# Performance work log

Hardware: AMD Instinct MI355X
Metric: run time of the kernel (lower is better)

Reference implementation:

```python
import jax, jax.numpy as jnp
import numpy as np

L, H, NH, V, T, B, K = 12, 768, 12, 30522, 512, 4, 21
DH = H // NH
INV_SQRT_DH = 1.0 / float(np.sqrt(DH))
NEG = -1e4  # BERT additive mask value
LN_EPS = 1e-12


def _ln(x, g, b):
    m = x.mean(-1, keepdims=True)
    v = jnp.var(x, axis=-1, keepdims=True)
    return (x - m) * jax.lax.rsqrt(v + LN_EPS) * g + b


def _encoder(input_ids, attention_mask, word_emb, pos_emb, tok_emb, emb_g, emb_b,
             Wqkv, bqkv, Wo, bo, ln1_g, ln1_b, W1, b1, W2, b2, ln2_g, ln2_b):
    Bv, Tv = input_ids.shape
    h = word_emb[input_ids] + pos_emb[None, :Tv] + tok_emb[0]  # token_type_ids = 0
    h = _ln(h, emb_g, emb_b)
    bias = (1.0 - attention_mask[:, None, None, :].astype(h.dtype)) * NEG  # [B,1,1,T]

    def layer(h, xs):
        wqkv, bq, wo, bo_, g1, b1_, w1, bb1, w2, bb2, g2, b2_ = xs
        qkv = h @ wqkv + bq  # [B,T,3H]
        q, k, v = jnp.split(qkv, 3, axis=-1)
        def hd(x):
            return x.reshape(Bv, Tv, NH, DH).transpose(0, 2, 1, 3)
        q, k, v = hd(q), hd(k), hd(v)
        scores = jnp.einsum('bhqd,bhkd->bhqk', q, k) * INV_SQRT_DH + bias
        ctx = jnp.einsum('bhqk,bhkd->bhqd', jax.nn.softmax(scores, axis=-1), v)
        ctx = ctx.transpose(0, 2, 1, 3).reshape(Bv, Tv, H)
        h = _ln(h + ctx @ wo + bo_, g1, b1_)  # post-LN (BERT)
        ff = jax.nn.gelu(h @ w1 + bb1, approximate=False) @ w2 + bb2
        h = _ln(h + ff, g2, b2_)
        return h, None

    h, _ = jax.lax.scan(layer, h, (Wqkv, bqkv, Wo, bo, ln1_g, ln1_b, W1, b1, W2, b2, ln2_g, ln2_b))
    return h


def _crf_nll(emissions, tags, mask, start, end, trans):
    # emissions [B,T,K], tags [B,T] int, mask [B,T] bool; torchcrf reduction='mean'
    Bv, Tv, Kv = emissions.shape
    maskf = mask.astype(emissions.dtype)
    # numerator: score of the gold path
    num = start[tags[:, 0]] + emissions[jnp.arange(Bv), 0, tags[:, 0]]
    em_t = jnp.take_along_axis(emissions, tags[..., None], axis=-1)[..., 0]  # [B,T]
    tr_t = trans[tags[:, :-1], tags[:, 1:]]  # [B,T-1]
    num = num + jnp.sum((tr_t + em_t[:, 1:]) * maskf[:, 1:], axis=1)
    last_idx = mask.sum(axis=1).astype(jnp.int32) - 1
    last_tag = jnp.take_along_axis(tags, last_idx[:, None], axis=1)[:, 0]
    num = num + end[last_tag]
    # denominator: forward algorithm (logsumexp recursion over time)
    alpha0 = start[None, :] + emissions[:, 0]  # [B,K]

    def step(alpha, xs):
        em, m = xs  # em [B,K], m [B] bool
        nxt = jax.scipy.special.logsumexp(alpha[:, :, None] + trans[None] + em[:, None, :], axis=1)
        return jnp.where(m[:, None], nxt, alpha), None

    alpha, _ = jax.lax.scan(step, alpha0, (emissions[:, 1:].transpose(1, 0, 2), mask[:, 1:].T))
    den = jax.scipy.special.logsumexp(alpha + end[None, :], axis=1)
    return -(num - den).mean()


def _viterbi(emissions, mask, start, end, trans):
    # Returns [B,T] int32 best paths; padded tail repeats the last valid tag.
    Bv, Tv, Kv = emissions.shape
    score0 = start[None, :] + emissions[:, 0]
    ident = jnp.broadcast_to(jnp.arange(Kv), (Bv, Kv))

    def step(score, xs):
        em, m = xs
        cand = score[:, :, None] + trans[None]  # [B,K_prev,K_next]
        idx = jnp.where(m[:, None], jnp.argmax(cand, axis=1), ident)
        nxt = jnp.max(cand, axis=1) + em
        return jnp.where(m[:, None], nxt, score), idx

    score, hist = jax.lax.scan(step, score0, (emissions[:, 1:].transpose(1, 0, 2), mask[:, 1:].T))
    last = jnp.argmax(score + end[None, :], axis=1)  # [B]

    def back(nxt_tag, idx):
        prev = jnp.take_along_axis(idx, nxt_tag[:, None], axis=1)[:, 0]
        return prev, nxt_tag

    tag0, rest = jax.lax.scan(back, last, hist, reverse=True)  # rest[i] = tag at t=i+1
    return jnp.concatenate([tag0[None], rest], axis=0).T.astype(jnp.int32)


def setup_inputs():
    key = jax.random.key(0)
    ks = jax.random.split(key, 16)
    s = 0.02

    def n(k, shape):
        return (s * jax.random.normal(k, shape)).astype(jnp.float32)

    def u(k, shape):
        return jax.random.uniform(k, shape, minval=-0.1, maxval=0.1).astype(jnp.float32)

    p = {}
    p['input_ids'] = jax.random.randint(ks[0], (B, T), 0, V)
    lengths = jax.random.randint(ks[1], (B,), T // 2, T + 1)
    p['attention_mask'] = (jnp.arange(T)[None, :] < lengths[:, None]).astype(jnp.int32)
    p['valid_mask'] = p['attention_mask']
    p['labels'] = jax.random.randint(ks[2], (B, T), 0, K)
    p['word_emb'] = n(ks[3], (V, H))
    p['pos_emb'] = n(ks[4], (T, H))
    p['tok_emb'] = n(ks[5], (2, H))
    p['emb_g'] = jnp.ones((H,), jnp.float32)
    p['emb_b'] = jnp.zeros((H,), jnp.float32)
    p['Wqkv'] = n(ks[6], (L, H, 3 * H))
    p['bqkv'] = jnp.zeros((L, 3 * H), jnp.float32)
    p['Wo'] = n(ks[7], (L, H, H))
    p['bo'] = jnp.zeros((L, H), jnp.float32)
    p['ln1_g'] = jnp.ones((L, H), jnp.float32)
    p['ln1_b'] = jnp.zeros((L, H), jnp.float32)
    p['W1'] = n(ks[8], (L, H, 4 * H))
    p['b1'] = jnp.zeros((L, 4 * H), jnp.float32)
    p['W2'] = n(ks[9], (L, 4 * H, H))
    p['b2'] = jnp.zeros((L, H), jnp.float32)
    p['ln2_g'] = jnp.ones((L, H), jnp.float32)
    p['ln2_b'] = jnp.zeros((L, H), jnp.float32)
    p['Wc'] = n(ks[10], (H, K))
    p['bc'] = jnp.zeros((K,), jnp.float32)
    p['crf_start'] = u(ks[11], (K,))
    p['crf_end'] = u(ks[12], (K,))
    p['crf_trans'] = u(ks[13], (K, K))
    return p


def reference(input_ids, attention_mask, valid_mask, labels,
              word_emb, pos_emb, tok_emb, emb_g, emb_b,
              Wqkv, bqkv, Wo, bo, ln1_g, ln1_b, W1, b1, W2, b2, ln2_g, ln2_b,
              Wc, bc, crf_start, crf_end, crf_trans):
    h = _encoder(input_ids, attention_mask, word_emb, pos_emb, tok_emb, emb_g, emb_b,
                 Wqkv, bqkv, Wo, bo, ln1_g, ln1_b, W1, b1, W2, b2, ln2_g, ln2_b)
    emissions = h @ Wc + bc  # dropout is identity in eval/reference mode
    mask = attention_mask.astype(bool)
    nll = _crf_nll(emissions, labels, mask, crf_start, crf_end, crf_trans)
    decoded = _viterbi(emissions, mask, crf_start, crf_end, crf_trans)
    return nll, decoded
```

## Files before the change

kernel.cpp:

```cpp
#include <hip/hip_runtime.h>
#include <math.h>

constexpr int NLAYER = 12;
constexpr int H = 768;
constexpr int NH = 12;
constexpr int DH = 64;
constexpr int T = 512;
constexpr int B = 4;
constexpr int K = 21;
constexpr int BT = B * T;
constexpr float NEGB = -10000.0f;
constexpr float LNEPS = 1e-12f;
constexpr float INV_SQRT_DH = 0.125f;

typedef __attribute__((ext_vector_type(8))) short bf16x8;
typedef __attribute__((ext_vector_type(4))) float f32x4;
typedef __attribute__((ext_vector_type(4))) unsigned short u16x4;

__device__ __forceinline__ float wave_sum_f(float v) {
#pragma unroll
  for (int off = 32; off > 0; off >>= 1) v += __shfl_xor(v, off);
  return v;
}
__device__ __forceinline__ int wave_sum_i(int v) {
#pragma unroll
  for (int off = 32; off > 0; off >>= 1) v += __shfl_xor(v, off);
  return v;
}
__device__ __forceinline__ float readlane_f(float v, int i) {
  return __uint_as_float(__builtin_amdgcn_readlane(__float_as_uint(v), i));
}
__device__ __forceinline__ unsigned short f32_bf16_rn(float x) {
  unsigned int u = __float_as_uint(x);
  u += 0x7fffu + ((u >> 16) & 1u);
  return (unsigned short)(u >> 16);
}
__device__ __forceinline__ void split_bf16(float x, unsigned short& h, unsigned short& l) {
  h = f32_bf16_rn(x);
  float hf = __uint_as_float((unsigned int)h << 16);
  l = f32_bf16_rn(x - hf);
}
__device__ __forceinline__ void block_reduce_sum2(float& s, float& q) {
  __shared__ float red[8];
  s = wave_sum_f(s);
  q = wave_sum_f(q);
  int lane = threadIdx.x & 63, wid = threadIdx.x >> 6;
  if (lane == 0) { red[wid] = s; red[4 + wid] = q; }
  __syncthreads();
  s = red[0] + red[1] + red[2] + red[3];
  q = red[4] + red[5] + red[6] + red[7];
}

__global__ __launch_bounds__(256) void embed_ln_kernel(
    const int* __restrict__ ids, const float* __restrict__ wemb,
    const float* __restrict__ pemb, const float* __restrict__ temb,
    const float* __restrict__ g, const float* __restrict__ bta,
    float* __restrict__ h, unsigned short* __restrict__ hh,
    unsigned short* __restrict__ hl) {
  int row = blockIdx.x;
  int t = row % T;
  int id = ids[row];
  const float* wp = wemb + (size_t)id * H;
  const float* pp = pemb + (size_t)t * H;
  float x[3];
  float s = 0.f, q = 0.f;
#pragma unroll
  for (int i = 0; i < 3; i++) {
    int c = threadIdx.x + i * 256;
    x[i] = wp[c] + pp[c] + temb[c];
    s += x[i];
    q += x[i] * x[i];
  }
  block_reduce_sum2(s, q);
  float mean = s * (1.0f / H);
  float var = q * (1.0f / H) - mean * mean;
  float inv = rsqrtf(var + LNEPS);
#pragma unroll
  for (int i = 0; i < 3; i++) {
    int c = threadIdx.x + i * 256;
    float y = (x[i] - mean) * inv * g[c] + bta[c];
    h[(size_t)row * H + c] = y;
    unsigned short yh, yl;
    split_bf16(y, yh, yl);
    hh[(size_t)row * H + c] = yh;
    hl[(size_t)row * H + c] = yl;
  }
}

__global__ __launch_bounds__(256) void add_ln_kernel(
    float* __restrict__ h, const float* __restrict__ add,
    const float* __restrict__ g, const float* __restrict__ bta,
    unsigned short* __restrict__ hh, unsigned short* __restrict__ hl) {
  int row = blockIdx.x;
  size_t base = (size_t)row * H;
  float x[3];
  float s = 0.f, q = 0.f;
#pragma unroll
  for (int i = 0; i < 3; i++) {
    int c = threadIdx.x + i * 256;
    x[i] = h[base + c] + add[base + c];
    s += x[i];
    q += x[i] * x[i];
  }
  block_reduce_sum2(s, q);
  float mean = s * (1.0f / H);
  float var = q * (1.0f / H) - mean * mean;
  float inv = rsqrtf(var + LNEPS);
#pragma unroll
  for (int i = 0; i < 3; i++) {
    int c = threadIdx.x + i * 256;
    float y = (x[i] - mean) * inv * g[c] + bta[c];
    h[base + c] = y;
    unsigned short yh, yl;
    split_bf16(y, yh, yl);
    hh[base + c] = yh;
    hl[base + c] = yl;
  }
}

__global__ __launch_bounds__(256) void wconv_kernel(
    const float* __restrict__ w0, const float* __restrict__ w1,
    const float* __restrict__ w2, const float* __restrict__ w3,
    unsigned short* __restrict__ Wth, unsigned short* __restrict__ Wtl) {
  __shared__ float tile[32][33];
  int bid = blockIdx.x;
  const float* src;
  int Kd, N, tk, tn;
  size_t off;
  if (bid < 1728) {
    src = w0; Kd = 768; N = 2304; tk = bid / 72; tn = bid % 72; off = 0;
  } else if (bid < 2304) {
    int t2 = bid - 1728; src = w1; Kd = 768; N = 768; tk = t2 / 24; tn = t2 % 24;
    off = 1769472;
  } else if (bid < 4608) {
    int t2 = bid - 2304; src = w2; Kd = 768; N = 3072; tk = t2 / 96; tn = t2 % 96;
    off = 2359296;
  } else {
    int t2 = bid - 4608; src = w3; Kd = 3072; N = 768; tk = t2 / 24; tn = t2 % 24;
    off = 4718592;
  }
  int tid = threadIdx.x;
  int k0 = tk * 32, n0 = tn * 32;
  int r = tid >> 3, c = (tid & 7) * 4;
  float4 v = *(const float4*)(src + (size_t)(k0 + r) * N + n0 + c);
  tile[r][c + 0] = v.x; tile[r][c + 1] = v.y; tile[r][c + 2] = v.z; tile[r][c + 3] = v.w;
  __syncthreads();
  u16x4 hv, lv;
#pragma unroll
  for (int q2 = 0; q2 < 4; q2++) {
    unsigned short sh, sl;
    split_bf16(tile[c + q2][r], sh, sl);
    hv[q2] = sh; lv[q2] = sl;
  }
  size_t dst = off + (size_t)(n0 + r) * Kd + k0 + c;
  *(u16x4*)(Wth + dst) = hv;
  *(u16x4*)(Wtl + dst) = lv;
}

template <int BN, bool GELU, bool SPLITOUT>
__global__ __launch_bounds__(256) void gemm_bf3_kernel(
    const unsigned short* __restrict__ Ah, const unsigned short* __restrict__ Al,
    const unsigned short* __restrict__ Wth, const unsigned short* __restrict__ Wtl,
    const float* __restrict__ bias, float* __restrict__ C,
    unsigned short* __restrict__ Ch, unsigned short* __restrict__ Cl,
    int N, int Kd) {
  constexpr int WN = BN / 2;
  constexpr int FN = WN / 16;
  constexpr int AW = 128 * 32;
  constexpr int WW = BN * 32;
  __shared__ short lds_s[2 * AW + 2 * WW];
  int tid = threadIdx.x;
  int lane = tid & 63, wid = tid >> 6;
  int wr = wid >> 1, wc = wid & 1;
  int bm = blockIdx.y * 128, bn = blockIdx.x * BN;
  f32x4 acc[4][FN] = {};
  int lrow = lane >> 2, lslot = lane & 3;

  const unsigned short* sbase;
  int rowbase, ldsoff, nchunks;
  if (wid == 0)      { sbase = Ah;  rowbase = bm; ldsoff = 0;            nchunks = 8; }
  else if (wid == 1) { sbase = Al;  rowbase = bm; ldsoff = AW;           nchunks = 8; }
  else if (wid == 2) { sbase = Wth; rowbase = bn; ldsoff = 2 * AW;       nchunks = BN / 16; }
  else               { sbase = Wtl; rowbase = bn; ldsoff = 2 * AW + WW;  nchunks = BN / 16; }

  for (int k0 = 0; k0 < Kd; k0 += 32) {
#pragma unroll
    for (int c = 0; c < 8; c++) {
      if (c < nchunks) {
        const unsigned short* src =
            sbase + (size_t)(rowbase + c * 16 + lrow) * Kd + k0 + lslot * 8;
        char* dst = ((char*)lds_s) + ldsoff * 2 + c * 1024 + lane * 16;
        __builtin_amdgcn_global_load_lds(
            (const __attribute__((address_space(1))) void*)src,
            (__attribute__((address_space(3))) void*)dst, 16, 0, 0);
      }
    }
    __syncthreads();
    int lr = lane & 15, lg = lane >> 4;
    bf16x8 af_h[4], af_l[4], wf_h[FN], wf_l[FN];
#pragma unroll
    for (int i = 0; i < 4; i++) {
      int e = (wr * 64 + i * 16 + lr) * 32 + lg * 8;
      af_h[i] = *(const bf16x8*)&lds_s[e];
      af_l[i] = *(const bf16x8*)&lds_s[AW + e];
    }
#pragma unroll
    for (int j = 0; j < FN; j++) {
      int e = (wc * WN + j * 16 + lr) * 32 + lg * 8;
      wf_h[j] = *(const bf16x8*)&lds_s[2 * AW + e];
      wf_l[j] = *(const bf16x8*)&lds_s[2 * AW + WW + e];
    }
#pragma unroll
    for (int i = 0; i < 4; i++)
#pragma unroll
      for (int j = 0; j < FN; j++) {
        acc[i][j] = __builtin_amdgcn_mfma_f32_16x16x32_bf16(af_h[i], wf_h[j], acc[i][j], 0, 0, 0);
        acc[i][j] = __builtin_amdgcn_mfma_f32_16x16x32_bf16(af_l[i], wf_h[j], acc[i][j], 0, 0, 0);
        acc[i][j] = __builtin_amdgcn_mfma_f32_16x16x32_bf16(af_h[i], wf_l[j], acc[i][j], 0, 0, 0);
      }
    __syncthreads();
  }
  int lr = lane & 15, lg = lane >> 4;
#pragma unroll
  for (int i = 0; i < 4; i++) {
#pragma unroll
    for (int j = 0; j < FN; j++) {
      int row = bm + wr * 64 + i * 16 + lg * 4;
      int col = bn + wc * WN + j * 16 + lr;
      float bv = bias[col];
#pragma unroll
      for (int r = 0; r < 4; r++) {
        float v = acc[i][j][r] + bv;
        if (GELU) v = 0.5f * v * (1.0f + erff(v * 0.70710678118654752f));
        if (SPLITOUT) {
          unsigned short sh, sl;
          split_bf16(v, sh, sl);
          Ch[(size_t)(row + r) * N + col] = sh;
          Cl[(size_t)(row + r) * N + col] = sl;
        } else {
          C[(size_t)(row + r) * N + col] = v;
        }
      }
    }
  }
}

__global__ __launch_bounds__(256) void qk_kernel(
    const float* __restrict__ qkv, const int* __restrict__ mask,
    float* __restrict__ S) {
  int bh = blockIdx.z;
  int b = bh / NH, hh = bh % NH;
  int i0 = blockIdx.y * 64, j0 = blockIdx.x * 64;
  __shared__ float Qs[64][64];
  __shared__ float Ks[64][64];
  int tid = threadIdx.x;
  int r = tid >> 2;
  int cseg = (tid & 3) * 16;
  const float* qbase = qkv + (size_t)(b * T + i0 + r) * (3 * H) + hh * DH;
  const float* kbase = qkv + (size_t)(b * T + j0 + r) * (3 * H) + H + hh * DH;
#pragma unroll
  for (int ss = 0; ss < 4; ss++) {
    int c = cseg + ss * 4;
    float4 qa = *(const float4*)(qbase + c);
    float4 ka = *(const float4*)(kbase + c);
    Qs[c + 0][r] = qa.x; Qs[c + 1][r] = qa.y; Qs[c + 2][r] = qa.z; Qs[c + 3][r] = qa.w;
    Ks[c + 0][r] = ka.x; Ks[c + 1][r] = ka.y; Ks[c + 2][r] = ka.z; Ks[c + 3][r] = ka.w;
  }
  __syncthreads();
  int tx = tid & 15, ty = tid >> 4;
  float acc[4][4] = {};
#pragma unroll 4
  for (int d = 0; d < 64; d++) {
    float a_[4], b_[4];
    *(float4*)a_ = *(const float4*)&Qs[d][ty * 4];
    *(float4*)b_ = *(const float4*)&Ks[d][tx * 4];
#pragma unroll
    for (int i = 0; i < 4; i++)
#pragma unroll
      for (int j = 0; j < 4; j++)
        acc[i][j] = fmaf(a_[i], b_[j], acc[i][j]);
  }
  float bj[4];
#pragma unroll
  for (int q = 0; q < 4; q++)
    bj[q] = (1.0f - (float)mask[b * T + j0 + tx * 4 + q]) * NEGB;
#pragma unroll
  for (int i = 0; i < 4; i++) {
    int gi = i0 + ty * 4 + i;
    int gj = j0 + tx * 4;
    float4 o;
    o.x = acc[i][0] * INV_SQRT_DH + bj[0];
    o.y = acc[i][1] * INV_SQRT_DH + bj[1];
    o.z = acc[i][2] * INV_SQRT_DH + bj[2];
    o.w = acc[i][3] * INV_SQRT_DH + bj[3];
    *(float4*)(S + ((size_t)bh * T + gi) * T + gj) = o;
  }
}

__global__ __launch_bounds__(128) void softmax_kernel(float* __restrict__ S) {
  size_t row = blockIdx.x;
  float* p = S + row * T;
  int tid = threadIdx.x;
  float4 v = *(float4*)(p + tid * 4);
  float m = fmaxf(fmaxf(v.x, v.y), fmaxf(v.z, v.w));
#pragma unroll
  for (int off = 32; off > 0; off >>= 1) m = fmaxf(m, __shfl_xor(m, off));
  __shared__ float redm[2];
  __shared__ float reds[2];
  int wid = tid >> 6;
  if ((tid & 63) == 0) redm[wid] = m;
  __syncthreads();
  m = fmaxf(redm[0], redm[1]);
  v.x = __expf(v.x - m);
  v.y = __expf(v.y - m);
  v.z = __expf(v.z - m);
  v.w = __expf(v.w - m);
  float s = v.x + v.y + v.z + v.w;
  s = wave_sum_f(s);
  if ((tid & 63) == 0) reds[wid] = s;
  __syncthreads();
  s = reds[0] + reds[1];
  float inv = 1.0f / s;
  v.x *= inv; v.y *= inv; v.z *= inv; v.w *= inv;
  *(float4*)(p + tid * 4) = v;
}

__global__ __launch_bounds__(256) void pv_kernel(
    const float* __restrict__ S, const float* __restrict__ qkv,
    unsigned short* __restrict__ cth, unsigned short* __restrict__ ctl) {
  int bh = blockIdx.y;
  int b = bh / NH, hh = bh % NH;
  int i0 = blockIdx.x * 64;
  __shared__ float Ps[64][68];
  __shared__ float Vs[64][64];
  int tid = threadIdx.x;
  int r = tid >> 2;
  int cseg = (tid & 3) * 16;
  int tx = tid & 15, ty = tid >> 4;
  float acc[4][4] = {};
  const float* srow = S + ((size_t)bh * T + i0 + r) * T;
  const float* vbase = qkv + (size_t)(b * T) * (3 * H) + 2 * H + hh * DH;
  for (int k0 = 0; k0 < T; k0 += 64) {
    __syncthreads();
#pragma unroll
    for (int ss = 0; ss < 4; ss++) {
      int c = cseg + ss * 4;
      *(float4*)&Ps[r][c] = *(const float4*)(srow + k0 + c);
      *(float4*)&Vs[r][c] = *(const float4*)(vbase + (size_t)(k0 + r) * (3 * H) + c);
    }
    __syncthreads();
#pragma unroll
    for (int kk = 0; kk < 64; kk += 4) {
      float p_[4][4], v_[4][4];
#pragma unroll
      for (int i = 0; i < 4; i++)
        *(float4*)p_[i] = *(const float4*)&Ps[ty * 4 + i][kk];
#pragma unroll
      for (int s = 0; s < 4; s++)
        *(float4*)v_[s] = *(const float4*)&Vs[kk + s][tx * 4];
#pragma unroll
      for (int i = 0; i < 4; i++)
#pragma unroll
        for (int s = 0; s < 4; s++)
#pragma unroll
          for (int j = 0; j < 4; j++)
            acc[i][j] = fmaf(p_[i][s], v_[s][j], acc[i][j]);
    }
  }
#pragma unroll
  for (int i = 0; i < 4; i++) {
    int gi = i0 + ty * 4 + i;
    size_t idx = (size_t)(b * T + gi) * H + hh * DH + tx * 4;
    u16x4 hv, lv;
#pragma unroll
    for (int j = 0; j < 4; j++) {
      unsigned short sh, sl;
      split_bf16(acc[i][j], sh, sl);
      hv[j] = sh; lv[j] = sl;
    }
    *(u16x4*)(cth + idx) = hv;
    *(u16x4*)(ctl + idx) = lv;
  }
}

__global__ __launch_bounds__(256) void classifier_kernel(
    const float* __restrict__ h, const float* __restrict__ Wc,
    const float* __restrict__ bc, float* __restrict__ em) {
  int id = blockIdx.x * 256 + threadIdx.x;
  if (id >= BT * K) return;
  int row = id / K, k = id % K;
  float acc = bc[k];
  const float* hr = h + (size_t)row * H;
  for (int d = 0; d < H; d++) acc = fmaf(hr[d], Wc[d * K + k], acc);
  em[id] = acc;
}

#define MRG(vo, io, va, ia, vb, ib) \
  float vo = ((vb) > (va)) ? (vb) : (va); \
  int io = ((vb) > (va)) ? (ib) : (ia);

__global__ __launch_bounds__(64) void crf_fused_kernel(
    const float* __restrict__ em, const int* __restrict__ labels,
    const int* __restrict__ mask, const float* __restrict__ start,
    const float* __restrict__ endv, const float* __restrict__ trans,
    float* __restrict__ parts, float* __restrict__ outdec) {
  __shared__ float em_s[T * K];
  __shared__ int mask_s[T];
  __shared__ unsigned char hist_s[(T - 1) * K];
  __shared__ float sc_s[32];
  __shared__ __align__(16) float bcast[24];
  int b = blockIdx.x & 3;
  int role = blockIdx.x >> 2;
  int j = threadIdx.x;
  const float* eb = em + (size_t)b * T * K;
  for (int i = j; i < T * K / 4; i += 64)
    ((float4*)em_s)[i] = ((const float4*)eb)[i];
  for (int i = j; i < T; i += 64) mask_s[i] = mask[b * T + i];
  __syncthreads();
  bool act = (j < K);
  float tr[K];
#pragma unroll
  for (int i = 0; i < K; i++) tr[i] = act ? trans[i * K + j] : 0.f;

  if (role == 0) {
    const int* tb = labels + b * T;
    float numloc = 0.f;
    int cnt = 0;
    for (int t = j; t < T; t += 64) {
      cnt += mask_s[t];
      if (t >= 1 && mask_s[t]) {
        int tp = tb[t - 1], tc = tb[t];
        numloc += trans[tp * K + tc] + em_s[t * K + tc];
      }
    }
    float num = wave_sum_f(numloc);
    int cnttot = wave_sum_i(cnt);
    float etr[K];
#pragma unroll
    for (int i = 0; i < K; i++) etr[i] = __expf(tr[i]);
    float alpha = act ? (start[j] + em_s[j]) : 0.f;
    for (int t = 1; t < T; t++) {
      if (!mask_s[t]) continue;
      float m0 = readlane_f(alpha, 0);
      float ee = __expf(alpha - m0);
      if (act) bcast[j] = ee;
      __syncthreads();
      float4 B0 = *(const float4*)&bcast[0];
      float4 B1 = *(const float4*)&bcast[4];
      float4 B2 = *(const float4*)&bcast[8];
      float4 B3 = *(const float4*)&bcast[12];
      float4 B4 = *(const float4*)&bcast[16];
      float B20 = bcast[20];
      float a0 = fmaf(B4.x, etr[16], fmaf(B3.x, etr[12], fmaf(B2.x, etr[8], fmaf(B1.x, etr[4], B0.x * etr[0]))));
      float a1 = fmaf(B4.y, etr[17], fmaf(B3.y, etr[13], fmaf(B2.y, etr[9], fmaf(B1.y, etr[5], B0.y * etr[1]))));
      float a2 = fmaf(B4.z, etr[18], fmaf(B3.z, etr[14], fmaf(B2.z, etr[10], fmaf(B1.z, etr[6], B0.z * etr[2]))));
      float a3 = fmaf(B4.w, etr[19], fmaf(B3.w, etr[15], fmaf(B2.w, etr[11], fmaf(B1.w, etr[7], B0.w * etr[3]))));
      float ssum = fmaf(B20, etr[20], (a0 + a1) + (a2 + a3));
      float nxt = __logf(ssum) + m0 + (act ? em_s[t * K + j] : 0.f);
      if (act) alpha = nxt;
      __syncthreads();
    }
    float aj = act ? (alpha + endv[j]) : -3.0e38f;
    float mm = aj;
#pragma unroll
    for (int off = 32; off > 0; off >>= 1) mm = fmaxf(mm, __shfl_xor(mm, off));
    float e2 = act ? __expf(aj - mm) : 0.f;
    float s2 = wave_sum_f(e2);
    float den = __logf(s2) + mm;
    if (j == 0) {
      int tag0 = tb[0];
      int lastidx = cnttot - 1;
      float numtot = num + start[tag0] + em_s[tag0] + endv[tb[lastidx]];
      parts[b] = numtot - den;
    }
  } else {
    float score = act ? (start[j] + em_s[j]) : 0.f;
    for (int t = 1; t < T; t++) {
      int mk = mask_s[t];
      if (mk) {
        if (act) bcast[j] = score;
        __syncthreads();
        float4 B0 = *(const float4*)&bcast[0];
        float4 B1 = *(const float4*)&bcast[4];
        float4 B2 = *(const float4*)&bcast[8];
        float4 B3 = *(const float4*)&bcast[12];
        float4 B4 = *(const float4*)&bcast[16];
        float B20 = bcast[20];
        float c0 = B0.x + tr[0],  c1 = B0.y + tr[1],  c2 = B0.z + tr[2],  c3 = B0.w + tr[3];
        float c4 = B1.x + tr[4],  c5 = B1.y + tr[5],  c6 = B1.z + tr[6],  c7 = B1.w + tr[7];
        float c8 = B2.x + tr[8],  c9 = B2.y + tr[9],  c10 = B2.z + tr[10], c11 = B2.w + tr[11];
        float c12 = B3.x + tr[12], c13 = B3.y + tr[13], c14 = B3.z + tr[14], c15 = B3.w + tr[15];
        float c16 = B4.x + tr[16], c17 = B4.y + tr[17], c18 = B4.z + tr[18], c19 = B4.w + tr[19];
        float c20 = B20 + tr[20];
        MRG(m0v, m0i, c0, 0, c1, 1)
        MRG(m1v, m1i, c2, 2, c3, 3)
        MRG(m2v, m2i, c4, 4, c5, 5)
        MRG(m3v, m3i, c6, 6, c7, 7)
        MRG(m4v, m4i, c8, 8, c9, 9)
        MRG(m5v, m5i, c10, 10, c11, 11)
        MRG(m6v, m6i, c12, 12, c13, 13)
        MRG(m7v, m7i, c14, 14, c15, 15)
        MRG(m8v, m8i, c16, 16, c17, 17)
        MRG(m9v, m9i, c18, 18, c19, 19)
        MRG(p0v, p0i, m0v, m0i, m1v, m1i)
        MRG(p1v, p1i, m2v, m2i, m3v, m3i)
        MRG(p2v, p2i, m4v, m4i, m5v, m5i)
        MRG(p3v, p3i, m6v, m6i, m7v, m7i)
        MRG(p4v, p4i, m8v, m8i, m9v, m9i)
        MRG(r0v, r0i, p0v, p0i, p1v, p1i)
        MRG(r1v, r1i, p2v, p2i, p3v, p3i)
        MRG(r2v, r2i, p4v, p4i, c20, 20)
        MRG(s0v, s0i, r0v, r0i, r1v, r1i)
        MRG(fv, fi, s0v, s0i, r2v, r2i)
        if (act) {
          hist_s[(t - 1) * K + j] = (unsigned char)fi;
          score = fv + em_s[t * K + j];
        }
        __syncthreads();
      } else if (act) {
        hist_s[(t - 1) * K + j] = (unsigned char)j;
      }
    }
    if (act) sc_s[j] = score + endv[j];
    __syncthreads();
    if (j == 0) {
      float best = -3.0e38f;
      int cur = 0;
#pragma unroll
      for (int i = 0; i < K; i++)
        if (sc_s[i] > best) { best = sc_s[i]; cur = i; }
      outdec[b * T + (T - 1)] = (float)cur;
      for (int t = T - 1; t >= 1; t--) {
        cur = hist_s[(t - 1) * K + cur];
        outdec[b * T + (t - 1)] = (float)cur;
      }
    }
  }
}

__global__ void nll_final_kernel(const float* __restrict__ parts,
                                 float* __restrict__ out) {
  out[0] = -0.25f * (parts[0] + parts[1] + parts[2] + parts[3]);
}

extern "C" void kernel_launch(void* const* d_in, const int* in_sizes, int n_in,
                              void* d_out, int out_size, void* d_ws, size_t ws_size,
                              hipStream_t stream) {
  (void)in_sizes; (void)n_in; (void)out_size; (void)ws_size;
  const int* ids    = (const int*)d_in[0];
  const int* amask  = (const int*)d_in[1];
  const int* labels = (const int*)d_in[3];
  const float* wemb = (const float*)d_in[4];
  const float* pemb = (const float*)d_in[5];
  const float* temb = (const float*)d_in[6];
  const float* eg   = (const float*)d_in[7];
  const float* ebta = (const float*)d_in[8];
  const float* Wqkv = (const float*)d_in[9];
  const float* bqkv = (const float*)d_in[10];
  const float* Wo   = (const float*)d_in[11];
  const float* bo   = (const float*)d_in[12];
  const float* ln1g = (const float*)d_in[13];
  const float* ln1b = (const float*)d_in[14];
  const float* W1   = (const float*)d_in[15];
  const float* b1   = (const float*)d_in[16];
  const float* W2   = (const float*)d_in[17];
  const float* b2   = (const float*)d_in[18];
  const float* ln2g = (const float*)d_in[19];
  const float* ln2b = (const float*)d_in[20];
  const float* Wc   = (const float*)d_in[21];
  const float* bc   = (const float*)d_in[22];
  const float* cst  = (const float*)d_in[23];
  const float* cen  = (const float*)d_in[24];
  const float* ctr  = (const float*)d_in[25];
  float* out = (float*)d_out;

  float* ws = (float*)d_ws;
  float* h    = ws;
  unsigned short* hh = (unsigned short*)(h + 1572864);
  unsigned short* hl = (unsigned short*)(h + 1572864 + 786432);
  float* qkv  = h + 1572864 + 786432 * 2;
  unsigned short* cth = (unsigned short*)(qkv + 4718592);
  unsigned short* ctl = (unsigned short*)(qkv + 4718592 + 786432);
  float* tmp  = qkv + 4718592 + 786432 * 2;
  float* big  = tmp + 1572864;
  unsigned short* gh = (unsigned short*)(big + 12582912);
  unsigned short* gl = (unsigned short*)(big + 12582912 + 3145728);
  unsigned short* Wth = (unsigned short*)(big + 12582912 + 3145728 * 2);
  unsigned short* Wtl = (unsigned short*)(big + 12582912 + 3145728 * 2 + 3538944);
  float* em   = big + 12582912 + 3145728 * 2 + 3538944 * 2;
  float* parts = em + 43008;

  embed_ln_kernel<<<BT, 256, 0, stream>>>(ids, wemb, pemb, temb, eg, ebta, h, hh, hl);

  for (int l = 0; l < NLAYER; l++) {
    const float* bqkv_l = bqkv + (size_t)l * 3 * H;
    const float* bo_l   = bo + (size_t)l * H;
    const float* b1_l   = b1 + (size_t)l * 4 * H;
    const float* b2_l   = b2 + (size_t)l * H;

    wconv_kernel<<<6912, 256, 0, stream>>>(
        Wqkv + (size_t)l * H * 3 * H, Wo + (size_t)l * H * H,
        W1 + (size_t)l * H * 4 * H, W2 + (size_t)l * 4 * H * H, Wth, Wtl);

    gemm_bf3_kernel<128, false, false><<<dim3(18, 16), 256, 0, stream>>>(
        hh, hl, Wth, Wtl, bqkv_l, qkv, nullptr, nullptr, 3 * H, H);
    qk_kernel<<<dim3(T / 64, T / 64, B * NH), 256, 0, stream>>>(qkv, amask, big);
    softmax_kernel<<<B * NH * T, 128, 0, stream>>>(big);
    pv_kernel<<<dim3(T / 64, B * NH), 256, 0, stream>>>(big, qkv, cth, ctl);
    gemm_bf3_kernel<64, false, false><<<dim3(12, 16), 256, 0, stream>>>(
        cth, ctl, Wth + 1769472, Wtl + 1769472, bo_l, tmp, nullptr, nullptr, H, H);
    add_ln_kernel<<<BT, 256, 0, stream>>>(h, tmp, ln1g + (size_t)l * H, ln1b + (size_t)l * H, hh, hl);
    gemm_bf3_kernel<128, true, true><<<dim3(24, 16), 256, 0, stream>>>(
        hh, hl, Wth + 2359296, Wtl + 2359296, b1_l, nullptr, gh, gl, 4 * H, H);
    gemm_bf3_kernel<64, false, false><<<dim3(12, 16), 256, 0, stream>>>(
        gh, gl, Wth + 4718592, Wtl + 4718592, b2_l, tmp, nullptr, nullptr, H, 4 * H);
    add_ln_kernel<<<BT, 256, 0, stream>>>(h, tmp, ln2g + (size_t)l * H, ln2b + (size_t)l * H, hh, hl);
  }

  classifier_kernel<<<(BT * K + 255) / 256, 256, 0, stream>>>(h, Wc, bc, em);
  crf_fused_kernel<<<8, 64, 0, stream>>>(em, labels, amask, cst, cen, ctr, parts, out + 1);
  nll_final_kernel<<<1, 1, 0, stream>>>(parts, out);
}
```

Before: 3.727 ms.

## Double-buffer GEMM LDS staging and replace CRF LDS broadcasts with readlane

The bf16x3 GEMM now double-buffers its LDS tiles. It issues the global-to-LDS loads for the next k-step before computing the current one and uses vmcnt waits with raw barriers, so load latency overlaps MFMA work. In the CRF forward and Viterbi recursions, the per-step LDS broadcast and two block barriers are replaced by register readlanes within the single wave, which shortens the serial dependency chain. The costs are doubled LDS use per GEMM block, which may lower occupancy, and hand-tuned vmcnt counts that must match the number of issued loads per wave.

```diff
diff --git a/kernel.cpp b/kernel.cpp
--- a/kernel.cpp
+++ b/kernel.cpp
@@ -16,6 +16,8 @@
 typedef __attribute__((ext_vector_type(8))) short bf16x8;
 typedef __attribute__((ext_vector_type(4))) float f32x4;
 typedef __attribute__((ext_vector_type(4))) unsigned short u16x4;
+
+#define WAIT_VMCNT(n) asm volatile("s_waitcnt vmcnt(" #n ")")
 
 __device__ __forceinline__ float wave_sum_f(float v) {
 #pragma unroll
@@ -168,7 +170,8 @@
   constexpr int FN = WN / 16;
   constexpr int AW = 128 * 32;
   constexpr int WW = BN * 32;
-  __shared__ short lds_s[2 * AW + 2 * WW];
+  constexpr int DBS = 2 * AW + 2 * WW;
+  __shared__ short lds_s[2 * DBS];
   int tid = threadIdx.x;
   int lane = tid & 63, wid = tid >> 6;
   int wr = wid >> 1, wc = wid & 1;
@@ -183,32 +186,49 @@
   else if (wid == 2) { sbase = Wth; rowbase = bn; ldsoff = 2 * AW;       nchunks = BN / 16; }
   else               { sbase = Wtl; rowbase = bn; ldsoff = 2 * AW + WW;  nchunks = BN / 16; }
 
-  for (int k0 = 0; k0 < Kd; k0 += 32) {
+  const unsigned short* srcbase = sbase + (size_t)(rowbase + lrow) * Kd + lslot * 8;
+
+  auto STAGE = [&](int db, int k0) {
 #pragma unroll
     for (int c = 0; c < 8; c++) {
       if (c < nchunks) {
-        const unsigned short* src =
-            sbase + (size_t)(rowbase + c * 16 + lrow) * Kd + k0 + lslot * 8;
-        char* dst = ((char*)lds_s) + ldsoff * 2 + c * 1024 + lane * 16;
+        const unsigned short* src = srcbase + (size_t)(c * 16) * Kd + k0;
+        char* dst = ((char*)lds_s) + (db * DBS + ldsoff) * 2 + c * 1024 + lane * 16;
         __builtin_amdgcn_global_load_lds(
             (const __attribute__((address_space(1))) void*)src,
             (__attribute__((address_space(3))) void*)dst, 16, 0, 0);
       }
     }
-    __syncthreads();
+  };
+
+  const int NT = Kd / 32;
+  STAGE(0, 0);
+  for (int kt = 0; kt < NT; kt++) {
+    int cur = kt & 1;
+    bool more = (kt + 1 < NT);
+    if (more) STAGE(cur ^ 1, (kt + 1) * 32);
+    if (more) {
+      if (BN == 128 || wid < 2) { WAIT_VMCNT(8); } else { WAIT_VMCNT(4); }
+    } else {
+      WAIT_VMCNT(0);
+    }
+    __builtin_amdgcn_s_barrier();
+    __builtin_amdgcn_sched_barrier(0);
+
     int lr = lane & 15, lg = lane >> 4;
+    int cb = cur * DBS;
     bf16x8 af_h[4], af_l[4], wf_h[FN], wf_l[FN];
 #pragma unroll
     for (int i = 0; i < 4; i++) {
       int e = (wr * 64 + i * 16 + lr) * 32 + lg * 8;
-      af_h[i] = *(const bf16x8*)&lds_s[e];
-      af_l[i] = *(const bf16x8*)&lds_s[AW + e];
+      af_h[i] = *(const bf16x8*)&lds_s[cb + e];
+      af_l[i] = *(const bf16x8*)&lds_s[cb + AW + e];
     }
 #pragma unroll
     for (int j = 0; j < FN; j++) {
       int e = (wc * WN + j * 16 + lr) * 32 + lg * 8;
-      wf_h[j] = *(const bf16x8*)&lds_s[2 * AW + e];
-      wf_l[j] = *(const bf16x8*)&lds_s[2 * AW + WW + e];
+      wf_h[j] = *(const bf16x8*)&lds_s[cb + 2 * AW + e];
+      wf_l[j] = *(const bf16x8*)&lds_s[cb + 2 * AW + WW + e];
     }
 #pragma unroll
     for (int i = 0; i < 4; i++)
@@ -218,8 +238,12 @@
         acc[i][j] = __builtin_amdgcn_mfma_f32_16x16x32_bf16(af_l[i], wf_h[j], acc[i][j], 0, 0, 0);
         acc[i][j] = __builtin_amdgcn_mfma_f32_16x16x32_bf16(af_h[i], wf_l[j], acc[i][j], 0, 0, 0);
       }
-    __syncthreads();
-  }
+    asm volatile("s_waitcnt lgkmcnt(0)");
+    __builtin_amdgcn_sched_barrier(0);
+    __builtin_amdgcn_s_barrier();
+    __builtin_amdgcn_sched_barrier(0);
+  }
+
   int lr = lane & 15, lg = lane >> 4;
 #pragma unroll
   for (int i = 0; i < 4; i++) {
@@ -408,7 +432,6 @@
   __shared__ int mask_s[T];
   __shared__ unsigned char hist_s[(T - 1) * K];
   __shared__ float sc_s[32];
-  __shared__ __align__(16) float bcast[24];
   int b = blockIdx.x & 3;
   int role = blockIdx.x >> 2;
   int j = threadIdx.x;
@@ -443,29 +466,27 @@
       if (!mask_s[t]) continue;
       float m0 = readlane_f(alpha, 0);
       float ee = __expf(alpha - m0);
-      if (act) bcast[j] = ee;
-      __syncthreads();
-      float4 B0 = *(const float4*)&bcast[0];
-      float4 B1 = *(const float4*)&bcast[4];
-      float4 B2 = *(const float4*)&bcast[8];
-      float4 B3 = *(const float4*)&bcast[12];
-      float4 B4 = *(const float4*)&bcast[16];
-      float B20 = bcast[20];
-      float a0 = fmaf(B4.x, etr[16], fmaf(B3.x, etr[12], fmaf(B2.x, etr[8], fmaf(B1.x, etr[4], B0.x * etr[0]))));
-      float a1 = fmaf(B4.y, etr[17], fmaf(B3.y, etr[13], fmaf(B2.y, etr[9], fmaf(B1.y, etr[5], B0.y * etr[1]))));
-      float a2 = fmaf(B4.z, etr[18], fmaf(B3.z, etr[14], fmaf(B2.z, etr[10], fmaf(B1.z, etr[6], B0.z * etr[2]))));
-      float a3 = fmaf(B4.w, etr[19], fmaf(B3.w, etr[15], fmaf(B2.w, etr[11], fmaf(B1.w, etr[7], B0.w * etr[3]))));
-      float ssum = fmaf(B20, etr[20], (a0 + a1) + (a2 + a3));
+      float e0 = readlane_f(ee, 0),  e1 = readlane_f(ee, 1),  e2 = readlane_f(ee, 2);
+      float e3 = readlane_f(ee, 3),  e4 = readlane_f(ee, 4),  e5 = readlane_f(ee, 5);
+      float e6 = readlane_f(ee, 6),  e7 = readlane_f(ee, 7),  e8 = readlane_f(ee, 8);
+      float e9 = readlane_f(ee, 9),  e10 = readlane_f(ee, 10), e11 = readlane_f(ee, 11);
+      float e12 = readlane_f(ee, 12), e13 = readlane_f(ee, 13), e14 = readlane_f(ee, 14);
+      float e15 = readlane_f(ee, 15), e16 = readlane_f(ee, 16), e17 = readlane_f(ee, 17);
+      float e18 = readlane_f(ee, 18), e19 = readlane_f(ee, 19), e20 = readlane_f(ee, 20);
+      float a0 = fmaf(e16, etr[16], fmaf(e12, etr[12], fmaf(e8, etr[8],  fmaf(e4, etr[4], e0 * etr[0]))));
+      float a1 = fmaf(e17, etr[17], fmaf(e13, etr[13], fmaf(e9, etr[9],  fmaf(e5, etr[5], e1 * etr[1]))));
+      float a2 = fmaf(e18, etr[18], fmaf(e14, etr[14], fmaf(e10, etr[10], fmaf(e6, etr[6], e2 * etr[2]))));
+      float a3 = fmaf(e19, etr[19], fmaf(e15, etr[15], fmaf(e11, etr[11], fmaf(e7, etr[7], e3 * etr[3]))));
+      float ssum = fmaf(e20, etr[20], (a0 + a1) + (a2 + a3));
       float nxt = __logf(ssum) + m0 + (act ? em_s[t * K + j] : 0.f);
       if (act) alpha = nxt;
-      __syncthreads();
     }
     float aj = act ? (alpha + endv[j]) : -3.0e38f;
     float mm = aj;
 #pragma unroll
     for (int off = 32; off > 0; off >>= 1) mm = fmaxf(mm, __shfl_xor(mm, off));
-    float e2 = act ? __expf(aj - mm) : 0.f;
-    float s2 = wave_sum_f(e2);
+    float e2v = act ? __expf(aj - mm) : 0.f;
+    float s2 = wave_sum_f(e2v);
     float den = __logf(s2) + mm;
     if (j == 0) {
       int tag0 = tb[0];
@@ -478,20 +499,17 @@
     for (int t = 1; t < T; t++) {
       int mk = mask_s[t];
       if (mk) {
-        if (act) bcast[j] = score;
-        __syncthreads();
-        float4 B0 = *(const float4*)&bcast[0];
-        float4 B1 = *(const float4*)&bcast[4];
-        float4 B2 = *(const float4*)&bcast[8];
-        float4 B3 = *(const float4*)&bcast[12];
-        float4 B4 = *(const float4*)&bcast[16];
-        float B20 = bcast[20];
-        float c0 = B0.x + tr[0],  c1 = B0.y + tr[1],  c2 = B0.z + tr[2],  c3 = B0.w + tr[3];
-        float c4 = B1.x + tr[4],  c5 = B1.y + tr[5],  c6 = B1.z + tr[6],  c7 = B1.w + tr[7];
-        float c8 = B2.x + tr[8],  c9 = B2.y + tr[9],  c10 = B2.z + tr[10], c11 = B2.w + tr[11];
-        float c12 = B3.x + tr[12], c13 = B3.y + tr[13], c14 = B3.z + tr[14], c15 = B3.w + tr[15];
-        float c16 = B4.x + tr[16], c17 = B4.y + tr[17], c18 = B4.z + tr[18], c19 = B4.w + tr[19];
-        float c20 = B20 + tr[20];
+        float c0 = readlane_f(score, 0) + tr[0],   c1 = readlane_f(score, 1) + tr[1];
+        float c2 = readlane_f(score, 2) + tr[2],   c3 = readlane_f(score, 3) + tr[3];
+        float c4 = readlane_f(score, 4) + tr[4],   c5 = readlane_f(score, 5) + tr[5];
+        float c6 = readlane_f(score, 6) + tr[6],   c7 = readlane_f(score, 7) + tr[7];
+        float c8 = readlane_f(score, 8) + tr[8],   c9 = readlane_f(score, 9) + tr[9];
+        float c10 = readlane_f(score, 10) + tr[10], c11 = readlane_f(score, 11) + tr[11];
+        float c12 = readlane_f(score, 12) + tr[12], c13 = readlane_f(score, 13) + tr[13];
+        float c14 = readlane_f(score, 14) + tr[14], c15 = readlane_f(score, 15) + tr[15];
+        float c16 = readlane_f(score, 16) + tr[16], c17 = readlane_f(score, 17) + tr[17];
+        float c18 = readlane_f(score, 18) + tr[18], c19 = readlane_f(score, 19) + tr[19];
+        float c20 = readlane_f(score, 20) + tr[20];
         MRG(m0v, m0i, c0, 0, c1, 1)
         MRG(m1v, m1i, c2, 2, c3, 3)
         MRG(m2v, m2i, c4, 4, c5, 5)
@@ -516,7 +534,6 @@
           hist_s[(t - 1) * K + j] = (unsigned char)fi;
           score = fv + em_s[t * K + j];
         }
-        __syncthreads();
       } else if (act) {
         hist_s[(t - 1) * K + j] = (unsigned char)j;
       }
```

Measured after the change: 3.354 ms. 10.0% less time.
